# Optimization experiments

Hardware: AMD Instinct MI355X
Metric: run time of the kernel (lower is better)

## Reference

```python
import jax, jax.numpy as jnp
import numpy as np

ANCHOR_SCALES = np.array([32.0, 64.0, 128.0, 256.0, 512.0], dtype=np.float32)
ANCHOR_RATIOS = np.array([1.0], dtype=np.float32)
FEATURE_STRIDE = 1.0
NMS_THRESHOLD = 0.7
MAX_DET = 300
NUM_CLASSES = 4
H = 40
W = 40
C_IN = 2048


def _conv(x, w, b):
    y = jax.lax.conv_general_dilated(x, w, (1, 1), 'SAME',
                                     dimension_numbers=('NHWC', 'HWIO', 'NHWC'))
    return y + b


def _anchor_boxes(deltas):
    # deltas: [N, 4] with N = H*W*A, anchor index fastest (channel-minor reshape)
    scales, ratios = np.meshgrid(ANCHOR_SCALES, ANCHOR_RATIOS)
    scales, ratios = scales.flatten(), ratios.flatten()
    w_base = (scales * np.sqrt(ratios)).astype(np.float32)   # [A]
    h_base = (scales / np.sqrt(ratios)).astype(np.float32)   # [A]
    A = w_base.shape[0]
    xc = (np.arange(W, dtype=np.float32) * FEATURE_STRIDE)
    yc = (np.arange(H, dtype=np.float32) * FEATURE_STRIDE)
    xc, yc = np.meshgrid(xc, yc)
    xc, yc = xc.flatten(), yc.flatten()                       # [H*W]
    w_full = jnp.asarray(np.tile(w_base, H * W))              # [N]
    h_full = jnp.asarray(np.tile(h_base, H * W))
    xc_full = jnp.asarray(np.repeat(xc, A))
    yc_full = jnp.asarray(np.repeat(yc, A))
    widths = jnp.exp(deltas[:, 2]) * w_full
    heights = jnp.exp(deltas[:, 3]) * h_full
    x_ctr = xc_full + deltas[:, 0] * FEATURE_STRIDE
    y_ctr = yc_full + deltas[:, 1] * FEATURE_STRIDE
    return jnp.stack([x_ctr - 0.5 * widths, y_ctr - 0.5 * heights,
                      x_ctr + 0.5 * widths, y_ctr + 0.5 * heights], axis=-1)


def _nms(boxes, scores):
    # Greedy sequential NMS over all N boxes, exactly as the source's Python loop.
    N = boxes.shape[0]
    order = jnp.argsort(-scores)
    b = boxes[order]                         # score-descending boxes (differentiable)
    bd = jax.lax.stop_gradient(b)            # indices are not differentiated
    x1, y1, x2, y2 = bd[:, 0], bd[:, 1], bd[:, 2], bd[:, 3]
    area = (x2 - x1) * (y2 - y1)             # [N]
    iw = jnp.maximum(0.0, jnp.minimum(x2[:, None], x2[None, :]) - jnp.maximum(x1[:, None], x1[None, :]))
    ih = jnp.maximum(0.0, jnp.minimum(y2[:, None], y2[None, :]) - jnp.maximum(y1[:, None], y1[None, :]))
    inter = iw * ih                          # [N, N]
    iou = inter / (area[:, None] + area[None, :] - inter)
    idx = jnp.arange(N)

    def body(i, keep):
        sup = (iou[i] >= NMS_THRESHOLD) & keep[i] & (idx > i)
        return keep & ~sup

    keep = jax.lax.stop_gradient(jax.lax.fori_loop(0, N, body, jnp.ones((N,), bool)))
    sel = jnp.argsort(~keep, stable=True)[:MAX_DET]   # kept boxes first, score order preserved
    valid = keep[sel]
    rois = b[sel] * valid[:, None].astype(b.dtype)    # pad invalid slots with zeros
    return rois, valid


def setup_inputs() -> dict:
    key = jax.random.key(0)
    ks = jax.random.split(key, 8)
    def nrm(k, shape, s):
        return jax.random.normal(k, shape, dtype=jnp.float32) * s
    A = ANCHOR_SCALES.shape[0] * ANCHOR_RATIOS.shape[0]
    return {
        'features': jax.random.normal(ks[0], (1, H, W, C_IN), dtype=jnp.float32),
        'conv_w': nrm(ks[1], (3, 3, C_IN, 256), 0.01),
        'conv_b': jnp.zeros((256,), jnp.float32),
        'cls_w': nrm(ks[2], (1, 1, 256, 2 * A), 0.01),
        'cls_b': jnp.zeros((2 * A,), jnp.float32),
        'reg_w': nrm(ks[3], (1, 1, 256, 4 * A), 0.01),
        'reg_b': jnp.zeros((4 * A,), jnp.float32),
        'fc1_w': nrm(ks[4], (4, 1024), 0.05),
        'fc1_b': jnp.zeros((1024,), jnp.float32),
        'clsh_w': nrm(ks[5], (1024, NUM_CLASSES), 0.05),
        'clsh_b': jnp.zeros((NUM_CLASSES,), jnp.float32),
        'regh_w': nrm(ks[6], (1024, 4), 0.05),
        'regh_b': jnp.zeros((4,), jnp.float32),
    }


def reference(features, conv_w, conv_b, cls_w, cls_b, reg_w, reg_b,
              fc1_w, fc1_b, clsh_w, clsh_b, regh_w, regh_b):
    # RPN
    x = jax.nn.relu(_conv(features, conv_w, conv_b))                 # [1,H,W,256]
    logits = _conv(x, cls_w, cls_b).reshape(features.shape[0], -1, 2)  # [1,N,2]
    deltas = _conv(x, reg_w, reg_b).reshape(features.shape[0], -1, 4)  # [1,N,4]
    scores = jax.nn.softmax(logits, axis=-1)[0, :, 1]                # [N]
    boxes = _anchor_boxes(deltas[0])                                 # [N,4]
    # Sequential NMS -> ROIs
    rois, valid = _nms(boxes, scores)                                # [MAX_DET,4]
    # Classifier head on selected ROIs
    fc = jax.nn.relu(rois @ fc1_w + fc1_b)                           # [MAX_DET,1024]
    class_scores = jax.nn.softmax(fc @ clsh_w + clsh_b, axis=-1)     # [MAX_DET,NUM_CLASSES]
    box_deltas = fc @ regh_w + regh_b                                # [MAX_DET,4]
    return (class_scores, box_deltas, rois)
```

## Files before the change

kernel.cpp:

```cpp
#include <hip/hip_runtime.h>
#include <math.h>


#define H 40
#define W 40
#define CIN 2048
#define CMID 256
#define NBOX 8000
#define NCH 125
#define ROWW 128
#define MAXDET 300

typedef double d4 __attribute__((ext_vector_type(4)));

__global__ __launch_bounds__(512, 4) void conv3x3_kernel(
    const float* __restrict__ feat, const float* __restrict__ conv_w,
    double* __restrict__ xsum) {
  __shared__ double patch[4][42][33];
  const int t = threadIdx.x;
  const int blk = blockIdx.x;
  const int sk = blk & 31;
  const int nh = (blk >> 5) & 1;
  const int mt = blk >> 6;
  const int y0 = mt * 2;
  const int c0 = sk * 64;

  const int wave = t >> 6, lane = t & 63;
  const int nl = lane & 15;
  const int kk = lane >> 4;
  const int n1 = nh * 128 + wave * 16;

  d4 zero = (d4)0.0;
  double pa1 = (kk == 0) ? 1.0 : 0.0;
  double pb1 = (kk == 0) ? (double)nl : 0.0;
  d4 dcol = __builtin_amdgcn_mfma_f64_16x16x4f64(pa1, pb1, zero, 0, 0, 0);
  double pa2 = (kk == 0) ? (double)nl : 0.0;
  double pb2 = (kk == 0) ? 1.0 : 0.0;
  d4 drow = __builtin_amdgcn_mfma_f64_16x16x4f64(pa2, pb2, zero, 0, 0, 0);

  int apy[5], apx[5];
#pragma unroll
  for (int f = 0; f < 5; ++f) {
    int pos = f * 16 + nl;
    apy[f] = pos / 40;
    apx[f] = pos % 40;
  }

  d4 acc[5];
#pragma unroll
  for (int f = 0; f < 5; ++f) acc[f] = (d4)0.0;

  for (int s2 = 0; s2 < 2; ++s2) {
    const int ch = c0 + s2 * 32;
    if (s2) __syncthreads();
    for (int i = t; i < 4 * 42 * 32; i += 512) {
      int c = i & 31;
      int rc = i >> 5;
      int col = rc % 42;
      int row = rc / 42;
      int gy = y0 - 1 + row;
      int gx = col - 1;
      double v = 0.0;
      if (gy >= 0 && gy < H && gx >= 0 && gx < W)
        v = (double)feat[(gy * W + gx) * CIN + ch + c];
      patch[row][col][c] = v;
    }
    __syncthreads();

    for (int tap = 0; tap < 9; ++tap) {
      const int dy = tap / 3, dx = tap % 3;
      const double* ap0 = &patch[apy[0] + dy][apx[0] + dx][kk];
      const double* ap1 = &patch[apy[1] + dy][apx[1] + dx][kk];
      const double* ap2 = &patch[apy[2] + dy][apx[2] + dx][kk];
      const double* ap3 = &patch[apy[3] + dy][apx[3] + dx][kk];
      const double* ap4 = &patch[apy[4] + dy][apx[4] + dx][kk];
      const float* bp = conv_w + ((tap * CIN + ch + kk) * CMID + n1 + nl);
#pragma unroll
      for (int cq = 0; cq < 8; ++cq) {
        const int co = cq * 4;
        double b0 = (double)bp[co * CMID];
        double a0 = ap0[co];
        double a1 = ap1[co];
        double a2 = ap2[co];
        double a3 = ap3[co];
        double a4 = ap4[co];
        acc[0] = __builtin_amdgcn_mfma_f64_16x16x4f64(a0, b0, acc[0], 0, 0, 0);
        acc[1] = __builtin_amdgcn_mfma_f64_16x16x4f64(a1, b0, acc[1], 0, 0, 0);
        acc[2] = __builtin_amdgcn_mfma_f64_16x16x4f64(a2, b0, acc[2], 0, 0, 0);
        acc[3] = __builtin_amdgcn_mfma_f64_16x16x4f64(a3, b0, acc[3], 0, 0, 0);
        acc[4] = __builtin_amdgcn_mfma_f64_16x16x4f64(a4, b0, acc[4], 0, 0, 0);
      }
    }
  }

#pragma unroll
  for (int f = 0; f < 5; ++f)
#pragma unroll
    for (int i = 0; i < 4; ++i) {
      int pm = (int)drow[i];
      int pn = (int)dcol[i];
      int pos = f * 16 + pm;
      int py = pos / 40, px = pos % 40;
      int gpos = (y0 + py) * W + px;
      atomicAdd(&xsum[gpos * CMID + n1 + pn], acc[f][i]);
    }
}

__global__ __launch_bounds__(256) void heads_kernel(
    const double* __restrict__ xsum, const float* __restrict__ conv_b,
    const float* __restrict__ cls_w, const float* __restrict__ cls_b,
    const float* __restrict__ reg_w, const float* __restrict__ reg_b,
    double* __restrict__ scores, double* __restrict__ boxes) {
  __shared__ double xd[256];
  __shared__ double outv[32];
  const int p = blockIdx.x;
  const int t = threadIdx.x;
  double v = xsum[p * 256 + t] + (double)conv_b[t];
  xd[t] = v > 0.0 ? v : 0.0;
  __syncthreads();

  const int wave = t >> 6, lane = t & 63;
  for (int q = 0; q < 8; ++q) {
    int o = wave * 8 + q;
    if (o < 30) {
      double acc = 0.0;
      if (o < 10) {
#pragma unroll
        for (int k = 0; k < 4; ++k)
          acc += xd[lane * 4 + k] * (double)cls_w[(lane * 4 + k) * 10 + o];
      } else {
        int oo = o - 10;
#pragma unroll
        for (int k = 0; k < 4; ++k)
          acc += xd[lane * 4 + k] * (double)reg_w[(lane * 4 + k) * 20 + oo];
      }
#pragma unroll
      for (int off = 32; off > 0; off >>= 1) acc += __shfl_down(acc, off);
      if (lane == 0) outv[o] = acc;
    }
  }
  __syncthreads();

  if (t < 5) {
    const int a = t;
    double l0 = outv[2 * a] + (double)cls_b[2 * a];
    double l1 = outv[2 * a + 1] + (double)cls_b[2 * a + 1];
    double sc = 1.0 / (1.0 + exp(l0 - l1));
    const int n = p * 5 + a;
    scores[n] = sc;
    double d0 = outv[10 + 4 * a + 0] + (double)reg_b[4 * a + 0];
    double d1 = outv[10 + 4 * a + 1] + (double)reg_b[4 * a + 1];
    double d2 = outv[10 + 4 * a + 2] + (double)reg_b[4 * a + 2];
    double d3 = outv[10 + 4 * a + 3] + (double)reg_b[4 * a + 3];
    double scale = (double)(32 << a);
    double wdt = exp(d2) * scale;
    double hgt = exp(d3) * scale;
    double xc = (double)(p % W) + d0;
    double yc = (double)(p / W) + d1;
    boxes[n * 4 + 0] = xc - 0.5 * wdt;
    boxes[n * 4 + 1] = yc - 0.5 * hgt;
    boxes[n * 4 + 2] = xc + 0.5 * wdt;
    boxes[n * 4 + 3] = yc + 0.5 * hgt;
  }
}

__global__ __launch_bounds__(256) void rank_kernel(
    const double* __restrict__ scores, const double* __restrict__ boxes,
    double* __restrict__ bs, double* __restrict__ area) {
  const int gid = blockIdx.x * 256 + threadIdx.x;
  const int i = gid >> 5;
  const int js = gid & 31;
  if (i >= NBOX) return;
  const double si = scores[i];
  int cnt = 0;
  const int j0 = js * 250;
#pragma unroll 5
  for (int j = j0; j < j0 + 250; ++j) {
    double sj = scores[j];
    cnt += (sj > si || (sj == si && j < i)) ? 1 : 0;
  }
#pragma unroll
  for (int off = 16; off > 0; off >>= 1) cnt += __shfl_down(cnt, off, 32);
  if (js == 0) {
    double b0 = boxes[i * 4 + 0], b1 = boxes[i * 4 + 1];
    double b2 = boxes[i * 4 + 2], b3 = boxes[i * 4 + 3];
    bs[cnt * 4 + 0] = b0;
    bs[cnt * 4 + 1] = b1;
    bs[cnt * 4 + 2] = b2;
    bs[cnt * 4 + 3] = b3;
    area[cnt] = (b2 - b0) * (b3 - b1);
  }
}

__global__ __launch_bounds__(256) void iou_matrix_kernel(
    const double* __restrict__ bs, const double* __restrict__ area,
    unsigned long long* __restrict__ supmat) {
  __shared__ double jx1[64], jy1[64], jx2[64], jy2[64], ja[64];
  __shared__ double ix1[64], iy1[64], ix2[64], iy2[64], ia[64];
  const int ti = blockIdx.x / NCH, tj = blockIdx.x % NCH;
  if (tj < ti) return;
  const int t = threadIdx.x, wv = t >> 6, lane = t & 63;
  if (t < 64) {
    int j = tj * 64 + t;
    jx1[t] = bs[j * 4 + 0];
    jy1[t] = bs[j * 4 + 1];
    jx2[t] = bs[j * 4 + 2];
    jy2[t] = bs[j * 4 + 3];
    ja[t] = area[j];
  } else if (t < 128) {
    int l = t - 64;
    int i = ti * 64 + l;
    ix1[l] = bs[i * 4 + 0];
    iy1[l] = bs[i * 4 + 1];
    ix2[l] = bs[i * 4 + 2];
    iy2[l] = bs[i * 4 + 3];
    ia[l] = area[i];
  }
  __syncthreads();
  const double x1 = jx1[lane], y1 = jy1[lane], x2 = jx2[lane], y2 = jy2[lane];
  const double aj = ja[lane];
  const int jglob = tj * 64 + lane;
#pragma unroll 4
  for (int s = 0; s < 16; ++s) {
    const int il = wv * 16 + s;
    const int i = ti * 64 + il;
    const double bx1 = ix1[il], by1 = iy1[il], bx2 = ix2[il], by2 = iy2[il];
    const double ai = ia[il];
    double iw = fmin(x2, bx2) - fmax(x1, bx1);
    iw = iw > 0.0 ? iw : 0.0;
    double ih = fmin(y2, by2) - fmax(y1, by1);
    ih = ih > 0.0 ? ih : 0.0;
    double inter = iw * ih;
    bool sup = (jglob > i) && (inter >= 0.7 * (ai + aj - inter));
    unsigned long long wmask = __ballot(sup ? 1 : 0);
    if (lane == 0) supmat[(size_t)i * ROWW + tj] = wmask;
  }
}

__global__ __launch_bounds__(1024) void nms_serial_kernel(
    const double* __restrict__ bs,
    const unsigned long long* __restrict__ supmat,
    float* __restrict__ rois_out) {
  __shared__ unsigned long long mask[NCH];
  __shared__ int selK[MAXDET];
  __shared__ int kbl[2][64];
  __shared__ int kcnt_sh[2];
  __shared__ int nk_sh;
  const int t = threadIdx.x, lane = t & 63;

  for (int q = t; q < NCH; q += 1024) mask[q] = 0ull;
  if (t == 0) {
    kcnt_sh[0] = kcnt_sh[1] = 0;
    nk_sh = 0;
  }
  __syncthreads();

  unsigned long long wdiag = 0ull, wcrit = 0ull, crit = 0ull;
  if (t < 64) {
    wdiag = supmat[(size_t)lane * ROWW + 0];
    wcrit = supmat[(size_t)lane * ROWW + 1];
  }
  int nk = 0;
  for (int tc = 0; tc < NCH; ++tc) {
    const int par = tc & 1;
    if (t < 64) {
      unsigned long long m = mask[tc] | crit;
      unsigned long long cand = ~m;
      unsigned long long keptbits = 0ull;
      int cnt = 0;
      while (cand && nk < MAXDET) {
        int b = __ffsll(cand) - 1;
        unsigned long long bit = 1ull << b;
        keptbits |= bit;
        if (lane == 0) {
          selK[nk] = tc * 64 + b;
          kbl[par][cnt] = b;
        }
        cnt++;
        nk++;
        unsigned long long row = __shfl(wdiag, b);
        cand &= ~(row | bit);
      }
      unsigned long long v = ((keptbits >> lane) & 1ull) ? wcrit : 0ull;
#pragma unroll
      for (int off = 32; off > 0; off >>= 1) v |= __shfl_xor(v, off);
      crit = v;
      if (tc + 1 < NCH) {
        wdiag = supmat[(size_t)((tc + 1) * 64 + lane) * ROWW + (tc + 1)];
        wcrit = (tc + 2 < NCH)
                    ? supmat[(size_t)((tc + 1) * 64 + lane) * ROWW + (tc + 2)]
                    : 0ull;
      }
      if (lane == 0) {
        kcnt_sh[par] = cnt;
        nk_sh = nk;
      }
    } else if (tc > 0) {
      const int pp = par ^ 1;
      const int k = kcnt_sh[pp];
      const int ptc = tc - 1;
      const int w0 = ptc + 2;
      const int nwords = NCH - w0;
      if (k > 0 && nwords > 0) {
        const int npairs = k * nwords;
        for (int q = t - 64; q < npairs; q += 1024 - 64) {
          int b = kbl[pp][q / nwords];
          int w = w0 + q % nwords;
          unsigned long long r = supmat[(size_t)(ptc * 64 + b) * ROWW + w];
          if (r) {
            unsigned int* mw = (unsigned int*)&mask[w];
            unsigned int lo = (unsigned int)r;
            unsigned int hi = (unsigned int)(r >> 32);
            if (lo) atomicOr(&mw[0], lo);
            if (hi) atomicOr(&mw[1], hi);
          }
        }
      }
    }
    __syncthreads();
    nk = nk_sh;
    if (nk >= MAXDET) break;
  }
  __syncthreads();

  const int NK = nk < MAXDET ? nk : MAXDET;
  for (int r = t; r < MAXDET; r += 1024) {
    if (r < NK) {
      int p = selK[r];
      rois_out[r * 4 + 0] = (float)bs[p * 4 + 0];
      rois_out[r * 4 + 1] = (float)bs[p * 4 + 1];
      rois_out[r * 4 + 2] = (float)bs[p * 4 + 2];
      rois_out[r * 4 + 3] = (float)bs[p * 4 + 3];
    } else {
      rois_out[r * 4 + 0] = 0.f;
      rois_out[r * 4 + 1] = 0.f;
      rois_out[r * 4 + 2] = 0.f;
      rois_out[r * 4 + 3] = 0.f;
    }
  }
}

__global__ __launch_bounds__(256) void rcnn_head_kernel(
    const float* __restrict__ rois, const float* __restrict__ fc1_w,
    const float* __restrict__ fc1_b, const float* __restrict__ clsh_w,
    const float* __restrict__ clsh_b, const float* __restrict__ regh_w,
    const float* __restrict__ regh_b, float* __restrict__ out) {
  __shared__ float red[256 * 8];
  const int r = blockIdx.x, t = threadIdx.x;
  const float r0 = rois[r * 4 + 0], r1 = rois[r * 4 + 1];
  const float r2 = rois[r * 4 + 2], r3 = rois[r * 4 + 3];
  float pc[4] = {0, 0, 0, 0}, pb[4] = {0, 0, 0, 0};
#pragma unroll
  for (int q = 0; q < 4; ++q) {
    int j = t * 4 + q;
    float f = r0 * fc1_w[j] + r1 * fc1_w[1024 + j] + r2 * fc1_w[2048 + j] +
              r3 * fc1_w[3072 + j] + fc1_b[j];
    f = fmaxf(f, 0.f);
#pragma unroll
    for (int c = 0; c < 4; ++c) {
      pc[c] += f * clsh_w[j * 4 + c];
      pb[c] += f * regh_w[j * 4 + c];
    }
  }
#pragma unroll
  for (int u = 0; u < 4; ++u) {
    red[t * 8 + u] = pc[u];
    red[t * 8 + 4 + u] = pb[u];
  }
  __syncthreads();
  for (int s = 128; s > 0; s >>= 1) {
    if (t < s) {
#pragma unroll
      for (int u = 0; u < 8; ++u) red[t * 8 + u] += red[(t + s) * 8 + u];
    }
    __syncthreads();
  }
  if (t == 0) {
    float lg[4];
    float m = -1e30f;
#pragma unroll
    for (int c = 0; c < 4; ++c) {
      lg[c] = red[c] + clsh_b[c];
      m = fmaxf(m, lg[c]);
    }
    float s = 0.f;
#pragma unroll
    for (int c = 0; c < 4; ++c) {
      lg[c] = expf(lg[c] - m);
      s += lg[c];
    }
#pragma unroll
    for (int c = 0; c < 4; ++c) out[r * 4 + c] = lg[c] / s;
#pragma unroll
    for (int k = 0; k < 4; ++k)
      out[1200 + r * 4 + k] = red[4 + k] + regh_b[k];
  }
}

extern "C" void kernel_launch(void* const* d_in, const int* in_sizes, int n_in,
                              void* d_out, int out_size, void* d_ws,
                              size_t ws_size, hipStream_t stream) {
  const float* feat = (const float*)d_in[0];
  const float* conv_w = (const float*)d_in[1];
  const float* conv_b = (const float*)d_in[2];
  const float* cls_w = (const float*)d_in[3];
  const float* cls_b = (const float*)d_in[4];
  const float* reg_w = (const float*)d_in[5];
  const float* reg_b = (const float*)d_in[6];
  const float* fc1_w = (const float*)d_in[7];
  const float* fc1_b = (const float*)d_in[8];
  const float* clsh_w = (const float*)d_in[9];
  const float* clsh_b = (const float*)d_in[10];
  const float* regh_w = (const float*)d_in[11];
  const float* regh_b = (const float*)d_in[12];
  float* out = (float*)d_out;

  char* w = (char*)d_ws;
  double* xsum = (double*)(w);
  double* scores = (double*)(w + 3276800);
  double* boxes = (double*)(w + 3340800);
  double* bs = (double*)(w + 3596800);
  double* area = (double*)(w + 3852800);
  unsigned long long* supmat =
      (unsigned long long*)(w + 3916800);

  hipMemsetAsync(xsum, 0, 3276800, stream);
  conv3x3_kernel<<<1280, 512, 0, stream>>>(feat, conv_w, xsum);
  heads_kernel<<<1600, 256, 0, stream>>>(xsum, conv_b, cls_w, cls_b, reg_w,
                                         reg_b, scores, boxes);
  rank_kernel<<<1000, 256, 0, stream>>>(scores, boxes, bs, area);
  iou_matrix_kernel<<<NCH * NCH, 256, 0, stream>>>(bs, area, supmat);
  nms_serial_kernel<<<1, 1024, 0, stream>>>(bs, supmat, out + 2400);
  rcnn_head_kernel<<<300, 256, 0, stream>>>(out + 2400, fc1_w, fc1_b, clsh_w,
                                            clsh_b, regh_w, regh_b, out);
}
```

Before: 551.8 us.

## Replace split-K atomics with per-slice partial buffers and launch only upper-triangle IoU tiles

When the workspace is large enough, each split-K conv block writes its partial sums to its own slice with plain stores. The heads kernel then reduces the 32 slices, which removes the fp64 atomicAdd contention and the memset. The IoU kernel now launches only the upper-triangular tile blocks and maps each block index back to (ti, tj) with a small loop, instead of launching the full grid and returning early. In exchange the partial path needs about 100 MB of extra workspace and many more reads in the heads kernel, and it is only taken if ws_size is large enough.

```diff
diff --git a/kernel.cpp b/kernel.cpp
--- a/kernel.cpp
+++ b/kernel.cpp
@@ -8,14 +8,16 @@
 #define CMID 256
 #define NBOX 8000
 #define NCH 125
+#define NTRI (NCH * (NCH + 1) / 2)
 #define ROWW 128
 #define MAXDET 300
+#define PSLICE 409600
 
 typedef double d4 __attribute__((ext_vector_type(4)));
 
 __global__ __launch_bounds__(512, 4) void conv3x3_kernel(
     const float* __restrict__ feat, const float* __restrict__ conv_w,
-    double* __restrict__ xsum) {
+    double* __restrict__ xsum, double* __restrict__ part, int use_part) {
   __shared__ double patch[4][42][33];
   const int t = threadIdx.x;
   const int blk = blockIdx.x;
@@ -93,21 +95,37 @@
     }
   }
 
-#pragma unroll
-  for (int f = 0; f < 5; ++f)
-#pragma unroll
-    for (int i = 0; i < 4; ++i) {
-      int pm = (int)drow[i];
-      int pn = (int)dcol[i];
-      int pos = f * 16 + pm;
-      int py = pos / 40, px = pos % 40;
-      int gpos = (y0 + py) * W + px;
-      atomicAdd(&xsum[gpos * CMID + n1 + pn], acc[f][i]);
-    }
+  if (use_part) {
+    double* dst = part + (size_t)sk * PSLICE;
+#pragma unroll
+    for (int f = 0; f < 5; ++f)
+#pragma unroll
+      for (int i = 0; i < 4; ++i) {
+        int pm = (int)drow[i];
+        int pn = (int)dcol[i];
+        int pos = f * 16 + pm;
+        int py = pos / 40, px = pos % 40;
+        int gpos = (y0 + py) * W + px;
+        dst[gpos * CMID + n1 + pn] = acc[f][i];
+      }
+  } else {
+#pragma unroll
+    for (int f = 0; f < 5; ++f)
+#pragma unroll
+      for (int i = 0; i < 4; ++i) {
+        int pm = (int)drow[i];
+        int pn = (int)dcol[i];
+        int pos = f * 16 + pm;
+        int py = pos / 40, px = pos % 40;
+        int gpos = (y0 + py) * W + px;
+        atomicAdd(&xsum[gpos * CMID + n1 + pn], acc[f][i]);
+      }
+  }
 }
 
 __global__ __launch_bounds__(256) void heads_kernel(
-    const double* __restrict__ xsum, const float* __restrict__ conv_b,
+    const double* __restrict__ xsum, const double* __restrict__ part,
+    int use_part, const float* __restrict__ conv_b,
     const float* __restrict__ cls_w, const float* __restrict__ cls_b,
     const float* __restrict__ reg_w, const float* __restrict__ reg_b,
     double* __restrict__ scores, double* __restrict__ boxes) {
@@ -115,7 +133,16 @@
   __shared__ double outv[32];
   const int p = blockIdx.x;
   const int t = threadIdx.x;
-  double v = xsum[p * 256 + t] + (double)conv_b[t];
+  double v;
+  if (use_part) {
+    double s = 0.0;
+    const double* pp = part + p * 256 + t;
+#pragma unroll
+    for (int sl = 0; sl < 32; ++sl) s += pp[(size_t)sl * PSLICE];
+    v = s + (double)conv_b[t];
+  } else {
+    v = xsum[p * 256 + t] + (double)conv_b[t];
+  }
   xd[t] = v > 0.0 ? v : 0.0;
   __syncthreads();
 
@@ -197,8 +224,13 @@
     unsigned long long* __restrict__ supmat) {
   __shared__ double jx1[64], jy1[64], jx2[64], jy2[64], ja[64];
   __shared__ double ix1[64], iy1[64], ix2[64], iy2[64], ia[64];
-  const int ti = blockIdx.x / NCH, tj = blockIdx.x % NCH;
-  if (tj < ti) return;
+  int u = blockIdx.x;
+  int ti = 0, base = 0;
+  while (u - base >= NCH - ti) {
+    base += NCH - ti;
+    ti++;
+  }
+  const int tj = ti + (u - base);
   const int t = threadIdx.x, wv = t >> 6, lane = t & 63;
   if (t < 64) {
     int j = tj * 64 + t;
@@ -423,13 +455,15 @@
   double* area = (double*)(w + 3852800);
   unsigned long long* supmat =
       (unsigned long long*)(w + 3916800);
-
-  hipMemsetAsync(xsum, 0, 3276800, stream);
-  conv3x3_kernel<<<1280, 512, 0, stream>>>(feat, conv_w, xsum);
-  heads_kernel<<<1600, 256, 0, stream>>>(xsum, conv_b, cls_w, cls_b, reg_w,
-                                         reg_b, scores, boxes);
+  double* part = (double*)(w + 12108800);
+  const int use_part = (ws_size >= (size_t)12108800 + 104857600ull) ? 1 : 0;
+
+  if (!use_part) hipMemsetAsync(xsum, 0, 3276800, stream);
+  conv3x3_kernel<<<1280, 512, 0, stream>>>(feat, conv_w, xsum, part, use_part);
+  heads_kernel<<<1600, 256, 0, stream>>>(xsum, part, use_part, conv_b, cls_w,
+                                         cls_b, reg_w, reg_b, scores, boxes);
   rank_kernel<<<1000, 256, 0, stream>>>(scores, boxes, bs, area);
-  iou_matrix_kernel<<<NCH * NCH, 256, 0, stream>>>(bs, area, supmat);
+  iou_matrix_kernel<<<NTRI, 256, 0, stream>>>(bs, area, supmat);
   nms_serial_kernel<<<1, 1024, 0, stream>>>(bs, supmat, out + 2400);
   rcnn_head_kernel<<<300, 256, 0, stream>>>(out + 2400, fc1_w, fc1_b, clsh_w,
                                             clsh_b, regh_w, regh_b, out);
```

After: 550.5 us. About the same (-0.2%).
